# Kernel tuning notes

Hardware: AMD Instinct MI355X
Metric: run time of the kernel (lower is better)

## Reference

```python
import jax, jax.numpy as jnp
import numpy as np
import math

H = 2048
N = 4
DT_MIN = 0.001
DT_MAX = 0.1


def _init_params(seed=0):
    rng = np.random.RandomState(seed)
    # log_dt ~ U(log dt_min, log dt_max)
    log_dt = rng.rand(H) * (math.log(DT_MAX) - math.log(DT_MIN)) + math.log(DT_MIN)
    # Skew-like tridiagonal S
    S = np.zeros((N, N))
    idx = np.arange(N)
    S[idx, idx] = -0.5
    S[idx[:-1], idx[:-1] + 1] = 5.0 * (np.arange(N - 1) + 1)
    S[idx[1:], idx[1:] - 1] = -5.0 * (np.arange(N - 1) + 1)
    S_diag = np.diagonal(S)
    A_real = np.broadcast_to(np.mean(S_diag) * np.ones_like(S_diag), (H, N)).copy()
    A_imag_1d, V = np.linalg.eigh(S * -1j)
    A_imag = np.broadcast_to(A_imag_1d, (H, N)).copy()
    log_A_real = np.log(-A_real)
    B = np.ones((H, N))
    C = np.zeros((H, N)); C[:, -1] = 1.0
    Vinv = V.conj().T
    CV = np.einsum('hm,mn->hn', C.astype(np.complex128), V)
    VinvB = np.einsum('mn,hn->hm', Vinv, B.astype(np.complex128))
    f32 = lambda a: jnp.asarray(a, dtype=jnp.float32)
    return dict(
        log_dt=f32(log_dt),
        log_A_real=f32(log_A_real),
        A_imag=f32(A_imag),
        VinvB_real=f32(VinvB.real), VinvB_imag=f32(VinvB.imag),
        CV_real=f32(CV.real), CV_imag=f32(CV.imag),
    )


def setup_inputs() -> dict:
    inp = _init_params(seed=0)
    inp['L'] = 4096
    return inp


def reference(log_dt, log_A_real, A_imag, VinvB_real, VinvB_imag, CV_real, CV_imag, L):
    A = -jnp.exp(log_A_real) + 1j * A_imag            # (H, N) complex
    B = VinvB_real + 1j * VinvB_imag                  # (H, N)
    C = CV_real + 1j * CV_imag                        # (H, N)
    dt = jnp.exp(log_dt)                              # (H,)
    Adt = A * dt[:, None]                             # (H, N)
    A_bar = jnp.exp(Adt)
    B_bar = (A_bar - 1.0) * B / A                     # (H, N)
    t = jnp.arange(L, dtype=jnp.float32)              # (L,)
    K = jnp.exp(Adt[:, :, None] * t)                  # (H, N, L) complex
    # CKB = Re[ sum_n C * B_bar * K ]
    CKB = jnp.einsum('hn,hnl->hl', C * B_bar, K).real # (H, L) float32
    return CKB
```

## Files before the change

### kernel.cpp

```cpp
#include <hip/hip_runtime.h>
#include <math.h>

struct c2 { float re, im; };
struct cd { double re, im; };

__device__ __forceinline__ c2 cmul(c2 a, c2 b) {
    return { a.re * b.re - a.im * b.im, a.re * b.im + a.im * b.re };
}
__device__ __forceinline__ cd cmuld(cd a, cd b) {
    return { a.re * b.re - a.im * b.im, a.re * b.im + a.im * b.re };
}

__global__ __launch_bounds__(256) void pmsn_ssm_kernel(
    const float* __restrict__ log_dt,
    const float* __restrict__ log_A_real,
    const float* __restrict__ A_imag,
    const float* __restrict__ VBr, const float* __restrict__ VBi,
    const float* __restrict__ CVr, const float* __restrict__ CVi,
    float* __restrict__ out, int L)
{
    const int h    = blockIdx.x;
    const int lane = threadIdx.x;
    const double dt = exp((double)log_dt[h]);

    c2 k[4];
    c2 Ab[4];
    c2 R[4];

    const unsigned e4 = 4u * (unsigned)lane;

#pragma unroll
    for (int n = 0; n < 4; ++n) {
        const int idx = h * 4 + n;
        const double ar  = -exp((double)log_A_real[idx]);
        const double ai  = (double)A_imag[idx];
        const double adr = ar * dt;
        const double adi = ai * dt;

        const double em = exp(adr);
        const cd Abar = { em * cos(adi), em * sin(adi) };

        const cd B   = { (double)VBr[idx], (double)VBi[idx] };
        const cd num = cmuld({ Abar.re - 1.0, Abar.im }, B);
        const double inv = 1.0 / (ar * ar + ai * ai);
        const cd Bbar = { (num.re * ar + num.im * ai) * inv,
                          (num.im * ar - num.re * ai) * inv };
        const cd C  = { (double)CVr[idx], (double)CVi[idx] };
        const cd cb = cmuld(C, Bbar);

        cd p  = { 1.0, 0.0 };
        cd sq = Abar;
#pragma unroll
        for (int b = 0; b < 10; ++b) {
            if (e4 & (1u << b)) p = cmuld(p, sq);
            sq = cmuld(sq, sq);
        }

        const cd k0 = cmuld(cb, p);
        k[n]  = { (float)k0.re,   (float)k0.im   };
        Ab[n] = { (float)Abar.re, (float)Abar.im };
        R[n]  = { (float)sq.re,   (float)sq.im   };
    }

    float4* outv = (float4*)(out + (size_t)h * (size_t)L);
    const int nIter = L >> 10;

    int vIdx = lane;
    for (int it = 0; it < nIter; ++it, vIdx += 256) {
        float4 v;
        c2 t[4];
        v.x = k[0].re + k[1].re + k[2].re + k[3].re;
#pragma unroll
        for (int n = 0; n < 4; ++n) t[n] = cmul(k[n], Ab[n]);
        v.y = t[0].re + t[1].re + t[2].re + t[3].re;
#pragma unroll
        for (int n = 0; n < 4; ++n) t[n] = cmul(t[n], Ab[n]);
        v.z = t[0].re + t[1].re + t[2].re + t[3].re;
#pragma unroll
        for (int n = 0; n < 4; ++n) t[n] = cmul(t[n], Ab[n]);
        v.w = t[0].re + t[1].re + t[2].re + t[3].re;

        outv[vIdx] = v;

#pragma unroll
        for (int n = 0; n < 4; ++n) k[n] = cmul(k[n], R[n]);
    }

    for (int l = (L & ~1023) + lane; l < L; l += 256) {
        double acc = 0.0;
#pragma unroll
        for (int n = 0; n < 4; ++n) {
            const int idx = h * 4 + n;
            const double ar  = -exp((double)log_A_real[idx]);
            const double ai  = (double)A_imag[idx];
            const double adr = ar * dt, adi = ai * dt;
            const double em = exp(adr);
            const cd Abar = { em * cos(adi), em * sin(adi) };
            const cd B   = { (double)VBr[idx], (double)VBi[idx] };
            const cd num = cmuld({ Abar.re - 1.0, Abar.im }, B);
            const double inv = 1.0 / (ar * ar + ai * ai);
            const cd Bbar = { (num.re * ar + num.im * ai) * inv,
                              (num.im * ar - num.re * ai) * inv };
            const cd C  = { (double)CVr[idx], (double)CVi[idx] };
            cd p = { 1.0, 0.0 }, sq = Abar;
            for (unsigned b = 0, ee = (unsigned)l; b < 13; ++b) {
                if (ee & (1u << b)) p = cmuld(p, sq);
                sq = cmuld(sq, sq);
            }
            const cd kk = cmuld(cmuld(C, Bbar), p);
            acc += kk.re;
        }
        out[(size_t)h * (size_t)L + l] = (float)acc;
    }
}

extern "C" void kernel_launch(void* const* d_in, const int* in_sizes, int n_in,
                              void* d_out, int out_size, void* d_ws, size_t ws_size,
                              hipStream_t stream) {
    const float* log_dt     = (const float*)d_in[0];
    const float* log_A_real = (const float*)d_in[1];
    const float* A_imag     = (const float*)d_in[2];
    const float* VBr        = (const float*)d_in[3];
    const float* VBi        = (const float*)d_in[4];
    const float* CVr        = (const float*)d_in[5];
    const float* CVi        = (const float*)d_in[6];
    float* out = (float*)d_out;

    const int H = in_sizes[0];
    const int L = out_size / H;

    pmsn_ssm_kernel<<<H, 256, 0, stream>>>(log_dt, log_A_real, A_imag,
                                           VBr, VBi, CVr, CVi, out, L);
}
```

Measured before the change: 101.5 us.

## Compute SSM per-mode setup once per block in shared memory, store nontemporally

Moves the double-precision per-mode setup (exp, sincos, B_bar, repeated squarings) from every thread to four threads per block and shares the results through shared memory. Each thread then builds its starting power in float by multiplying selected precomputed squares chosen by its lane bits. Output stores become nontemporal, and the tail loop is rewritten in float using the shared tables. This removes redundant FP64 transcendental and multiply work per thread, at the cost of a block barrier and less accurate float products. The tail path mishandles indices beyond the table (high bits treated as 1), though it does not run for L=4096.

```diff
diff --git a/kernel.cpp b/kernel.cpp
--- a/kernel.cpp
+++ b/kernel.cpp
@@ -3,6 +3,8 @@
 
 struct c2 { float re, im; };
 struct cd { double re, im; };
+
+typedef float f4 __attribute__((ext_vector_type(4)));
 
 __device__ __forceinline__ c2 cmul(c2 a, c2 b) {
     return { a.re * b.re - a.im * b.im, a.re * b.im + a.im * b.re };
@@ -21,17 +23,16 @@
 {
     const int h    = blockIdx.x;
     const int lane = threadIdx.x;
-    const double dt = exp((double)log_dt[h]);
 
-    c2 k[4];
-    c2 Ab[4];
-    c2 R[4];
+    __shared__ float sAb[4][2];
+    __shared__ float sR [4][2];
+    __shared__ float sCb[4][2];
+    __shared__ float sT [4][8][2];
 
-    const unsigned e4 = 4u * (unsigned)lane;
-
-#pragma unroll
-    for (int n = 0; n < 4; ++n) {
+    if (lane < 4) {
+        const int n   = lane;
         const int idx = h * 4 + n;
+        const double dt  = exp((double)log_dt[h]);
         const double ar  = -exp((double)log_A_real[idx]);
         const double ai  = (double)A_imag[idx];
         const double adr = ar * dt;
@@ -48,26 +49,42 @@
         const cd C  = { (double)CVr[idx], (double)CVi[idx] };
         const cd cb = cmuld(C, Bbar);
 
-        cd p  = { 1.0, 0.0 };
-        cd sq = Abar;
+        sAb[n][0] = (float)Abar.re; sAb[n][1] = (float)Abar.im;
+        sCb[n][0] = (float)cb.re;   sCb[n][1] = (float)cb.im;
+
+        cd sq = cmuld(Abar, Abar);
+        sq = cmuld(sq, sq);
 #pragma unroll
-        for (int b = 0; b < 10; ++b) {
-            if (e4 & (1u << b)) p = cmuld(p, sq);
+        for (int b = 0; b < 8; ++b) {
+            sT[n][b][0] = (float)sq.re; sT[n][b][1] = (float)sq.im;
             sq = cmuld(sq, sq);
         }
+        sR[n][0] = (float)sq.re; sR[n][1] = (float)sq.im;
+    }
+    __syncthreads();
 
-        const cd k0 = cmuld(cb, p);
-        k[n]  = { (float)k0.re,   (float)k0.im   };
-        Ab[n] = { (float)Abar.re, (float)Abar.im };
-        R[n]  = { (float)sq.re,   (float)sq.im   };
+    c2 k[4], Ab[4], R[4];
+#pragma unroll
+    for (int n = 0; n < 4; ++n) {
+        Ab[n] = { sAb[n][0], sAb[n][1] };
+        R [n] = { sR [n][0], sR [n][1] };
+        c2 p  = { sCb[n][0], sCb[n][1] };
+#pragma unroll
+        for (int b = 0; b < 8; ++b) {
+            const bool on = (lane >> b) & 1;
+            const c2 t = { on ? sT[n][b][0] : 1.0f,
+                           on ? sT[n][b][1] : 0.0f };
+            p = cmul(p, t);
+        }
+        k[n] = p;
     }
 
-    float4* outv = (float4*)(out + (size_t)h * (size_t)L);
+    f4* outv = (f4*)(out + (size_t)h * (size_t)L);
     const int nIter = L >> 10;
 
     int vIdx = lane;
     for (int it = 0; it < nIter; ++it, vIdx += 256) {
-        float4 v;
+        f4 v;
         c2 t[4];
         v.x = k[0].re + k[1].re + k[2].re + k[3].re;
 #pragma unroll
@@ -80,37 +97,31 @@
         for (int n = 0; n < 4; ++n) t[n] = cmul(t[n], Ab[n]);
         v.w = t[0].re + t[1].re + t[2].re + t[3].re;
 
-        outv[vIdx] = v;
+        __builtin_nontemporal_store(v, &outv[vIdx]);
 
 #pragma unroll
         for (int n = 0; n < 4; ++n) k[n] = cmul(k[n], R[n]);
     }
 
     for (int l = (L & ~1023) + lane; l < L; l += 256) {
-        double acc = 0.0;
+        float acc = 0.0f;
 #pragma unroll
         for (int n = 0; n < 4; ++n) {
-            const int idx = h * 4 + n;
-            const double ar  = -exp((double)log_A_real[idx]);
-            const double ai  = (double)A_imag[idx];
-            const double adr = ar * dt, adi = ai * dt;
-            const double em = exp(adr);
-            const cd Abar = { em * cos(adi), em * sin(adi) };
-            const cd B   = { (double)VBr[idx], (double)VBi[idx] };
-            const cd num = cmuld({ Abar.re - 1.0, Abar.im }, B);
-            const double inv = 1.0 / (ar * ar + ai * ai);
-            const cd Bbar = { (num.re * ar + num.im * ai) * inv,
-                              (num.im * ar - num.re * ai) * inv };
-            const cd C  = { (double)CVr[idx], (double)CVi[idx] };
-            cd p = { 1.0, 0.0 }, sq = Abar;
-            for (unsigned b = 0, ee = (unsigned)l; b < 13; ++b) {
-                if (ee & (1u << b)) p = cmuld(p, sq);
-                sq = cmuld(sq, sq);
+            c2 p = { sCb[n][0], sCb[n][1] };
+            const unsigned q = ((unsigned)l) >> 2;
+            const unsigned r = ((unsigned)l) & 3u;
+            for (unsigned b = 0; b < 11; ++b) {
+                if (q & (1u << b)) {
+                    const c2 t = (b < 8) ? c2{ sT[n][b][0], sT[n][b][1] }
+                                         : c2{ 1.0f, 0.0f };
+                    p = cmul(p, t);
+                }
             }
-            const cd kk = cmuld(cmuld(C, Bbar), p);
-            acc += kk.re;
+            const c2 Abn = { sAb[n][0], sAb[n][1] };
+            for (unsigned j = 0; j < r; ++j) p = cmul(p, Abn);
+            acc += p.re;
         }
-        out[(size_t)h * (size_t)L + l] = (float)acc;
+        out[(size_t)h * (size_t)L + l] = acc;
     }
 }
 
```

Measured after the change: 88.79 us. 1.14x faster.
